# Kernel tuning notes

Hardware: AMD Instinct MI355X
Metric: run time of the kernel (lower is better)

The kernel has to match this reference:

```python
import jax, jax.numpy as jnp
import numpy as np
import math

NEG = -1e9
B, TX, TY, ODIM = 32, 512, 2048, 80


def setup_inputs() -> dict:
    key = jax.random.key(0)
    k1, k2 = jax.random.split(key)
    return {
        "x_m": jax.random.normal(k1, (B, TX, ODIM), jnp.float32),
        "x_logs": jnp.zeros((B, TX, ODIM), jnp.float32),  # mean_only=True -> zeros_like(x_m)
        "z": jax.random.normal(k2, (B, ODIM, TY), jnp.float32),
        "x_mask": jnp.ones((B, 1, TX), jnp.float32),
        "z_mask": jnp.ones((B, 1, TY), jnp.float32),
    }


def maximum_path(logp, mask, tx_len, ty_len):
    """Monotonic alignment search (Glow-TTS Viterbi DP).
    logp: [B, Tx, Ty] log-likelihoods; mask: [B, Tx, Ty]; lengths: [B] int32.
    Returns hard alignment path [B, Tx, Ty] in {0,1}.
    """
    B_, Tx, Ty = logp.shape
    xs = jnp.arange(Tx)
    logp = jnp.where(mask > 0, logp, NEG)

    # Forward DP over mel frames y: f[x,y] = logp[x,y] + max(f[x-1,y-1], f[x,y-1])
    def fwd_step(prev, y):
        v_cur = jnp.where(xs[None, :] == y, NEG, prev)              # stay (invalid on diagonal)
        prev_shift = jnp.concatenate(
            [jnp.full((B_, 1), NEG, logp.dtype), prev[:, :-1]], axis=1)
        v_prev = jnp.where(xs[None, :] == 0,
                           jnp.where(y == 0, jnp.zeros((), logp.dtype), jnp.asarray(NEG, logp.dtype)),
                           prev_shift)                               # advance
        f = logp[:, :, y] + jnp.maximum(v_prev, v_cur)
        return f, f

    _, fcols = jax.lax.scan(fwd_step, jnp.full((B_, Tx), NEG, logp.dtype), jnp.arange(Ty))
    # fcols: [Ty, B, Tx]

    # Backtrack from (tx_len-1, ty_len-1) down to y=0.
    def bwd_step(index, y):
        active = y < ty_len                                          # [B] bool
        row = jax.nn.one_hot(index, Tx, dtype=logp.dtype) * active[:, None].astype(logp.dtype)
        fm1 = fcols[jnp.maximum(y - 1, 0)]                           # [B, Tx]
        f_here = jnp.take_along_axis(fm1, index[:, None], axis=1)[:, 0]
        f_left = jnp.take_along_axis(fm1, jnp.maximum(index - 1, 0)[:, None], axis=1)[:, 0]
        move = (index != 0) & ((index == y) | (f_here < f_left))
        new_index = jnp.where(active & move, index - 1, index)
        return new_index, row

    _, rows = jax.lax.scan(bwd_step, tx_len - 1, jnp.arange(Ty - 1, -1, -1))
    path = jnp.flip(rows, axis=0).transpose(1, 2, 0)                 # [B, Tx, Ty]
    return path * mask


def reference(x_m, x_logs, z, x_mask, z_mask):
    # attn_mask: [B, Tx, Ty]
    attn_mask = x_mask[:, 0, :, None] * z_mask[:, 0, None, :]

    # Gaussian log-likelihood of each frame z[:, :, y] under each text token's N(x_m, exp(x_logs))
    x_s_sq_r = jnp.exp(-2.0 * x_logs)                                # [B, Tx, D]
    logp1 = jnp.sum(-0.5 * math.log(2.0 * math.pi) - x_logs, axis=2)[:, :, None]
    logp2 = jnp.einsum('btd,bdy->bty', x_s_sq_r, -0.5 * z * z)
    logp3 = jnp.einsum('btd,bdy->bty', x_m * x_s_sq_r, z)
    logp4 = jnp.sum(-0.5 * x_m * x_m * x_s_sq_r, axis=2)[:, :, None]
    logp = logp1 + logp2 + logp3 + logp4                             # [B, Tx, Ty]

    tx_len = jnp.sum(x_mask[:, 0, :], axis=1).astype(jnp.int32)
    ty_len = jnp.sum(z_mask[:, 0, :], axis=1).astype(jnp.int32)
    attn = jax.lax.stop_gradient(
        maximum_path(jax.lax.stop_gradient(logp), attn_mask, tx_len, ty_len))

    # Expand token stats to frame level with the hard alignment.
    z_m = jnp.einsum('bxy,bxd->bdy', attn, x_m)                      # [B, D, Ty]
    z_logs = jnp.einsum('bxy,bxd->bdy', attn, x_logs)                # [B, D, Ty]
    log_durations_ = jnp.log(1e-8 + jnp.sum(attn, axis=-1))[:, None, :] * x_mask  # [B, 1, Tx]
    return z_m, z_logs, log_durations_, attn
```

## Files before the change

### kernel.cpp

```cpp
#include <hip/hip_runtime.h>
#include <math.h>

#define B_ 32
#define TX_ 512
#define TY_ 2048
#define D_ 80
#define NEG (-1e9f)
#define SEG 32

typedef float f32x4 __attribute__((ext_vector_type(4)));

#define GLB(p) ((const __attribute__((address_space(1))) void*)(p))
#define LDSP(p) ((__attribute__((address_space(3))) void*)(p))

__global__ __launch_bounds__(128) void prep_kernel(
    const float* __restrict__ x_m, const float* __restrict__ x_logs,
    float* __restrict__ Cc, int* __restrict__ flag)
{
    int row = blockIdx.x;
    int t = threadIdx.x;
    __shared__ float red[128];
    float contrib = 0.f;
    bool nz = false;
    if (t < D_) {
        float xl = x_logs[(size_t)row * D_ + t];
        float xm = x_m[(size_t)row * D_ + t];
        nz = (xl != 0.f);
        float a1 = expf(-2.f * xl);
        contrib = -0.91893853320467274178f - xl - 0.5f * xm * xm * a1;
    }
    unsigned long long m = __ballot(nz);
    if ((t & 63) == 0 && m) atomicOr(flag, 1);
    red[t] = contrib;
    __syncthreads();
    if (t < 64) {
        float v = red[t] + red[t + 64];
        #pragma unroll
        for (int off = 32; off >= 1; off >>= 1) v += __shfl_down(v, off);
        if (t == 0) Cc[row] = v;
    }
}

__global__ __launch_bounds__(256) void lens_kernel(const float* __restrict__ x_mask,
    const float* __restrict__ z_mask, int* __restrict__ lens)
{
    int blk = blockIdx.x; int t = threadIdx.x;
    __shared__ float red[256];
    float s = 0.f;
    if (blk < B_) {
        for (int i = t; i < TX_; i += 256) s += x_mask[(size_t)blk * TX_ + i];
    } else {
        int b = blk - B_;
        for (int i = t; i < TY_; i += 256) s += z_mask[(size_t)b * TY_ + i];
    }
    red[t] = s; __syncthreads();
    for (int off = 128; off >= 1; off >>= 1) {
        if (t < off) red[t] += red[t + off];
        __syncthreads();
    }
    if (t == 0) lens[blk] = (int)(red[0] + 0.5f);
}

__global__ __launch_bounds__(256) void gemm_zero(
    const int* __restrict__ flag,
    const float* __restrict__ x_m, const float* __restrict__ Cc,
    const float* __restrict__ z,
    const float* __restrict__ x_mask, const float* __restrict__ z_mask,
    float* __restrict__ logpT, int y0, int C)
{
    if (*flag != 0) return;
    __shared__ float xs[40][132];
    __shared__ float zs[40][132];
    int b = blockIdx.z;
    int x0 = blockIdx.x * 128;
    int cy0 = blockIdx.y * 128;
    int yy0 = y0 + cy0;
    int tid = threadIdx.x;
    int tm = tid & 15, tn = tid >> 4;
    float acc[8][8];
    float accz[8];
    #pragma unroll
    for (int i = 0; i < 8; ++i) {
        accz[i] = 0.f;
        #pragma unroll
        for (int j = 0; j < 8; ++j) acc[i][j] = 0.f;
    }

    for (int h = 0; h < 2; ++h) {
        if (h) __syncthreads();
        for (int i = tid; i < 128 * 40; i += 256) {
            int m = i / 40, d = i - m * 40;
            xs[d][m] = x_m[((size_t)(b * TX_ + x0 + m)) * D_ + h * 40 + d];
        }
        for (int i = tid; i < 40 * 128; i += 256) {
            int d = i >> 7, n = i & 127;
            zs[d][n] = z[((size_t)(b * D_ + h * 40 + d)) * TY_ + yy0 + n];
        }
        __syncthreads();
        #pragma unroll 4
        for (int k = 0; k < 40; ++k) {
            f32x4 a0 = *(const f32x4*)&xs[k][tm * 4];
            f32x4 a1 = *(const f32x4*)&xs[k][64 + tm * 4];
            f32x4 z0 = *(const f32x4*)&zs[k][tn * 4];
            f32x4 z1 = *(const f32x4*)&zs[k][64 + tn * 4];
            float av[8], zv[8];
            #pragma unroll
            for (int i = 0; i < 4; ++i) { av[i] = a0[i]; av[i+4] = a1[i]; zv[i] = z0[i]; zv[i+4] = z1[i]; }
            #pragma unroll
            for (int j = 0; j < 8; ++j) {
                accz[j] = fmaf(zv[j], zv[j], accz[j]);
                #pragma unroll
                for (int i = 0; i < 8; ++i)
                    acc[i][j] = fmaf(av[i], zv[j], acc[i][j]);
            }
        }
    }
    f32x4 ccA = *(const f32x4*)&Cc[(size_t)b * TX_ + x0 + tm * 4];
    f32x4 ccB = *(const f32x4*)&Cc[(size_t)b * TX_ + x0 + 64 + tm * 4];
    f32x4 xmA = *(const f32x4*)&x_mask[(size_t)b * TX_ + x0 + tm * 4];
    f32x4 xmB = *(const f32x4*)&x_mask[(size_t)b * TX_ + x0 + 64 + tm * 4];
    #pragma unroll
    for (int jj = 0; jj < 8; ++jj) {
        int n = (jj < 4) ? (tn * 4 + jj) : (64 + tn * 4 + (jj - 4));
        float zmv = z_mask[(size_t)b * TY_ + yy0 + n];
        float sz = -0.5f * accz[jj];
        f32x4 oA, oB;
        #pragma unroll
        for (int i = 0; i < 4; ++i) {
            float vA = acc[i][jj] + ccA[i] + sz;
            float vB = acc[i + 4][jj] + ccB[i] + sz;
            oA[i] = (xmA[i] * zmv > 0.f) ? vA : NEG;
            oB[i] = (xmB[i] * zmv > 0.f) ? vB : NEG;
        }
        float* orow = &logpT[((size_t)b * C + cy0 + n) * TX_ + x0];
        *(f32x4*)(orow + tm * 4) = oA;
        *(f32x4*)(orow + 64 + tm * 4) = oB;
    }
}

__global__ __launch_bounds__(256) void gemm_logp(
    const int* __restrict__ flag,
    const float* __restrict__ x_m, const float* __restrict__ x_logs,
    const float* __restrict__ Cc,
    const float* __restrict__ z, const float* __restrict__ x_mask, const float* __restrict__ z_mask,
    float* __restrict__ logpT, int y0, int C)
{
    if (*flag == 0) return;
    __shared__ float A1s[D_][72];
    __shared__ float A2s[D_][72];
    __shared__ float zs[D_][64];
    int b = blockIdx.z;
    int x0 = blockIdx.x * 64;
    int cy0 = blockIdx.y * 64;
    int yy0 = y0 + cy0;
    int tid = threadIdx.x;
    for (int i = tid; i < 64 * D_; i += 256) {
        int m = i / D_, d = i - m * D_;
        size_t ga = ((size_t)(b * TX_ + x0 + m)) * D_ + d;
        float xl = x_logs[ga], xm = x_m[ga];
        float a1 = expf(-2.f * xl);
        A1s[d][m] = a1;
        A2s[d][m] = xm * a1;
    }
    for (int i = tid; i < D_ * 64; i += 256) {
        int d = i >> 6, n = i & 63;
        zs[d][n] = z[((size_t)(b * D_ + d)) * TY_ + yy0 + n];
    }
    __syncthreads();
    int tm = tid & 15, tn = tid >> 4;
    float acc[4][4];
    #pragma unroll
    for (int i = 0; i < 4; ++i)
        #pragma unroll
        for (int j = 0; j < 4; ++j) acc[i][j] = 0.f;
    #pragma unroll 4
    for (int k = 0; k < D_; ++k) {
        f32x4 a1 = *(const f32x4*)&A1s[k][tm * 4];
        f32x4 a2 = *(const f32x4*)&A2s[k][tm * 4];
        f32x4 zv = *(const f32x4*)&zs[k][tn * 4];
        #pragma unroll
        for (int j = 0; j < 4; ++j) {
            float h = -0.5f * zv[j];
            #pragma unroll
            for (int i = 0; i < 4; ++i) {
                float tt = fmaf(h, a1[i], a2[i]);
                acc[i][j] = fmaf(zv[j], tt, acc[i][j]);
            }
        }
    }
    f32x4 cc = *(const f32x4*)&Cc[(size_t)b * TX_ + x0 + tm * 4];
    f32x4 xm = *(const f32x4*)&x_mask[(size_t)b * TX_ + x0 + tm * 4];
    #pragma unroll
    for (int j = 0; j < 4; ++j) {
        int n = tn * 4 + j;
        float zmv = z_mask[(size_t)b * TY_ + yy0 + n];
        f32x4 o;
        #pragma unroll
        for (int i = 0; i < 4; ++i) {
            float val = acc[i][j] + cc[i];
            o[i] = (xm[i] * zmv > 0.f) ? val : NEG;
        }
        *(f32x4*)&logpT[((size_t)b * C + cy0 + n) * TX_ + x0 + tm * 4] = o;
    }
}

__device__ __forceinline__ unsigned int dp_step(int y, int lane, const f32x4 la, const f32x4 lb,
    float (&f)[8], unsigned int laneMask)
{
    float lp8[8];
    #pragma unroll
    for (int i = 0; i < 4; ++i) { lp8[i] = la[i]; lp8[i + 4] = lb[i]; }
    float sh = __shfl_up(f[7], 1);
    float edge = (y == 0) ? 0.f : NEG;
    float pm0 = (lane == 0) ? edge : sh;
    bool lanehit = (lane == (y >> 3));
    int jeq = y & 7;
    unsigned int byt = 0u;
    #pragma unroll
    for (int j = 7; j >= 0; --j) {
        float pm = (j == 0) ? pm0 : f[j - 1];
        bool ceq = lanehit && (jeq == j);
        byt = byt * 2u + (((f[j] < pm) || ceq) ? 1u : 0u);
        float vc = ceq ? NEG : f[j];
        f[j] = lp8[j] + fmaxf(pm, vc);
    }
    return byt & laneMask;
}

__device__ __forceinline__ void stage_seg(const char* gbase, float (*dst)[TX_],
    int sw, int t0)
{
    for (int d = sw; d < 2 * SEG; d += 3) {
        int s = d >> 1, h = d & 1;
        const char* g = gbase + ((size_t)(t0 + s) * TX_ + h * 256) * 4;
        __builtin_amdgcn_global_load_lds(GLB(g), LDSP(&dst[s][h * 256]), 16, 0, 0);
    }
}

__global__ __launch_bounds__(256, 1) void dp_forward(const float* __restrict__ logpT,
    float* __restrict__ fsave, unsigned char* __restrict__ bits8, int y0, int C)
{
    __shared__ float buf[2][SEG][TX_];
    int b = blockIdx.x, tid = threadIdx.x;
    int w = tid >> 6, lane = tid & 63;
    const char* gbase = (const char*)(logpT + (size_t)b * C * TX_) + lane * 16;
    unsigned char* bp = bits8 + ((size_t)b * TY_ + y0) * 64 + lane;

    float f[8];
    unsigned int laneMask = (lane == 0) ? 0xFEu : 0xFFu;
    if (w == 0) {
        if (y0 == 0) {
            #pragma unroll
            for (int j = 0; j < 8; ++j) f[j] = NEG;
        } else {
            f32x4 fa = *(const f32x4*)(fsave + (size_t)b * TX_ + lane * 8);
            f32x4 fb = *(const f32x4*)(fsave + (size_t)b * TX_ + lane * 8 + 4);
            #pragma unroll
            for (int j = 0; j < 4; ++j) { f[j] = fa[j]; f[j + 4] = fb[j]; }
        }
    } else {
        #pragma unroll
        for (int j = 0; j < 8; ++j) f[j] = 0.f;
    }

    if (w > 0) {
        stage_seg(gbase, buf[0], w - 1, 0);
        asm volatile("s_waitcnt vmcnt(0)" ::: "memory");
    }
    __syncthreads();

    int nseg = C / SEG;
    for (int g = 0; g < nseg; ++g) {
        if (w == 0) {
            float (*cur)[TX_] = buf[g & 1];
            int t0 = g * SEG;
            #pragma unroll 8
            for (int s = 0; s < SEG; ++s) {
                f32x4 la = *(const f32x4*)&cur[s][lane * 8];
                f32x4 lb = *(const f32x4*)&cur[s][lane * 8 + 4];
                unsigned int byt = dp_step(y0 + t0 + s, lane, la, lb, f, laneMask);
                bp[(size_t)(t0 + s) * 64] = (unsigned char)byt;
            }
        } else {
            if (g + 1 < nseg) stage_seg(gbase, buf[(g + 1) & 1], w - 1, (g + 1) * SEG);
            asm volatile("s_waitcnt vmcnt(0)" ::: "memory");
        }
        __syncthreads();
    }

    if (w == 0) {
        f32x4 fa, fb;
        #pragma unroll
        for (int j = 0; j < 4; ++j) { fa[j] = f[j]; fb[j] = f[j + 4]; }
        *(f32x4*)(fsave + (size_t)b * TX_ + lane * 8) = fa;
        *(f32x4*)(fsave + (size_t)b * TX_ + lane * 8 + 4) = fb;
    }
}

__global__ __launch_bounds__(64) void backtrack_kernel(
    const unsigned char* __restrict__ bits8, const int* __restrict__ lens,
    const float* __restrict__ x_mask, int* __restrict__ idxA, float* __restrict__ logdur)
{
    int b = blockIdx.x, lane = threadIdx.x;
    __shared__ int durS[TX_];
    for (int x = lane; x < TX_; x += 64) durS[x] = 0;
    int tx_len = lens[b];
    int ty_len = lens[B_ + b];
    int idx = tx_len - 1;
    if (idx < 0) idx = 0;
    int cnt = 0;
    const unsigned long long* bu = (const unsigned long long*)(bits8 + (size_t)b * TY_ * 64);
    for (int w = 0; w < TY_ / 64; ++w) {
        int ytop = TY_ - 1 - w * 64;
        int yl = ytop - lane;
        int Whi = idx >> 6;
        unsigned long long whi = bu[(size_t)yl * 8 + Whi];
        unsigned long long wlo = (Whi > 0) ? bu[(size_t)yl * 8 + Whi - 1] : 0ull;
        int rec = -1;
        for (int s = 0; s < 64; ++s) {
            int y = ytop - s;
            bool active = (y < ty_len);
            if (lane == s) rec = active ? idx : -1;
            if (active) cnt++;
            unsigned long long wsel = ((idx >> 6) == Whi) ? __shfl(whi, s) : __shfl(wlo, s);
            int bit = (int)((wsel >> (idx & 63)) & 1ull);
            if (active && bit) {
                if (lane == 0) durS[idx] = cnt;
                cnt = 0;
                idx -= 1;
            }
        }
        idxA[(size_t)b * TY_ + yl] = rec;
    }
    if (lane == 0) durS[idx] = cnt;
    __syncthreads();
    for (int x = lane; x < TX_; x += 64) {
        float dv = (float)durS[x];
        logdur[(size_t)b * TX_ + x] = logf(1e-8f + dv) * x_mask[(size_t)b * TX_ + x];
    }
}

__global__ __launch_bounds__(256) void attn_write(const int* __restrict__ idxA,
    const float* __restrict__ x_mask, const float* __restrict__ z_mask,
    float* __restrict__ attn_o)
{
    int b = blockIdx.z; int x = blockIdx.y;
    int yq = blockIdx.x * 256 + threadIdx.x;
    int4 iv = ((const int4*)(idxA + (size_t)b * TY_))[yq];
    float xm = x_mask[(size_t)b * TX_ + x];
    float4 zm4 = ((const float4*)(z_mask + (size_t)b * TY_))[yq];
    float4 o;
    o.x = (iv.x == x) ? xm * zm4.x : 0.f;
    o.y = (iv.y == x) ? xm * zm4.y : 0.f;
    o.z = (iv.z == x) ? xm * zm4.z : 0.f;
    o.w = (iv.w == x) ? xm * zm4.w : 0.f;
    ((float4*)(attn_o + ((size_t)(b * TX_ + x)) * TY_))[yq] = o;
}

__global__ __launch_bounds__(256) void zm_write(const int* __restrict__ idxA,
    const float* __restrict__ x_m, const float* __restrict__ x_logs,
    const float* __restrict__ x_mask, const float* __restrict__ z_mask,
    float* __restrict__ z_m_o, float* __restrict__ z_logs_o)
{
    int b = blockIdx.z; int d = blockIdx.y;
    int yq = blockIdx.x * 256 + threadIdx.x;
    int4 iv = ((const int4*)(idxA + (size_t)b * TY_))[yq];
    float4 zm4 = ((const float4*)(z_mask + (size_t)b * TY_))[yq];
    float4 om, ol;
    float* omv = (float*)&om; float* olv = (float*)&ol;
    int ivv[4] = {iv.x, iv.y, iv.z, iv.w};
    float zmv[4] = {zm4.x, zm4.y, zm4.z, zm4.w};
    #pragma unroll
    for (int c = 0; c < 4; ++c) {
        float vm = 0.f, vl = 0.f;
        int ix = ivv[c];
        if (ix >= 0) {
            float wgt = x_mask[(size_t)b * TX_ + ix] * zmv[c];
            size_t ga = ((size_t)(b * TX_ + ix)) * D_ + d;
            vm = wgt * x_m[ga];
            vl = wgt * x_logs[ga];
        }
        omv[c] = vm; olv[c] = vl;
    }
    ((float4*)(z_m_o    + ((size_t)(b * D_ + d)) * TY_))[yq] = om;
    ((float4*)(z_logs_o + ((size_t)(b * D_ + d)) * TY_))[yq] = ol;
}

extern "C" void kernel_launch(void* const* d_in, const int* in_sizes, int n_in,
                              void* d_out, int out_size, void* d_ws, size_t ws_size,
                              hipStream_t stream)
{
    const float* x_m    = (const float*)d_in[0];
    const float* x_logs = (const float*)d_in[1];
    const float* z      = (const float*)d_in[2];
    const float* x_mask = (const float*)d_in[3];
    const float* z_mask = (const float*)d_in[4];
    float* out = (float*)d_out;
    float* z_m_o    = out;
    float* z_logs_o = out + (size_t)B_ * D_ * TY_;
    float* logdur_o = out + (size_t)2 * B_ * D_ * TY_;
    float* attn_o   = logdur_o + (size_t)B_ * TX_;

    char* p = (char*)d_ws;
    float* Cc = (float*)p;            p += (size_t)B_ * TX_ * 4;
    float* fs = (float*)p;            p += (size_t)B_ * TX_ * 4;
    unsigned char* bits8 = (unsigned char*)p; p += (size_t)B_ * TY_ * 64;
    int* idxA = (int*)p;              p += (size_t)B_ * TY_ * 4;
    int* lens = (int*)p;              p += 256;
    int* flag = (int*)p;              p += 256;
    float* logpC = (float*)p;
    size_t fixed = (size_t)(p - (char*)d_ws);
    size_t avail = (ws_size > fixed) ? (ws_size - fixed) : 0;
    int C = 128;
    const int cands[5] = {2048, 1024, 512, 256, 128};
    for (int i = 0; i < 5; ++i) {
        if ((size_t)B_ * cands[i] * TX_ * 4 <= avail) { C = cands[i]; break; }
    }

    hipMemsetAsync(flag, 0, sizeof(int), stream);
    prep_kernel<<<B_ * TX_, 128, 0, stream>>>(x_m, x_logs, Cc, flag);
    lens_kernel<<<2 * B_, 256, 0, stream>>>(x_mask, z_mask, lens);
    int nc = TY_ / C;
    for (int c = 0; c < nc; ++c) {
        gemm_zero<<<dim3(TX_ / 128, C / 128, B_), 256, 0, stream>>>(
            flag, x_m, Cc, z, x_mask, z_mask, logpC, c * C, C);
        gemm_logp<<<dim3(TX_ / 64, C / 64, B_), 256, 0, stream>>>(
            flag, x_m, x_logs, Cc, z, x_mask, z_mask, logpC, c * C, C);
        dp_forward<<<B_, 256, 0, stream>>>(logpC, fs, bits8, c * C, C);
    }
    backtrack_kernel<<<B_, 64, 0, stream>>>(bits8, lens, x_mask, idxA, logdur_o);
    attn_write<<<dim3(TY_ / 4 / 256, TX_, B_), 256, 0, stream>>>(idxA, x_mask, z_mask, attn_o);
    zm_write<<<dim3(TY_ / 4 / 256, D_, B_), 256, 0, stream>>>(
        idxA, x_m, x_logs, x_mask, z_mask, z_m_o, z_logs_o);
}
```

Measured before the change: 761.5 us.

## Stride DP columns across lanes and emit direction bits via wave ballots

The forward DP's cell-to-lane mapping changes from 8 contiguous cells per lane to a strided mapping where lane l owns cells j*64+l. Each step now rotates all 8 register values across lanes with shuffles. This removes the serial 8-deep max chain inside each lane, and the direction bits come from ballots, written as 8 64-bit words by 8 lanes instead of 64 byte stores. The bit layout in memory stays what the backtrack kernel expects. The cost is 8 cross-lane permutes per step instead of 1, plus ballot overhead.

```diff
diff --git a/kernel.cpp b/kernel.cpp
--- a/kernel.cpp
+++ b/kernel.cpp
@@ -204,29 +204,6 @@
     }
 }
 
-__device__ __forceinline__ unsigned int dp_step(int y, int lane, const f32x4 la, const f32x4 lb,
-    float (&f)[8], unsigned int laneMask)
-{
-    float lp8[8];
-    #pragma unroll
-    for (int i = 0; i < 4; ++i) { lp8[i] = la[i]; lp8[i + 4] = lb[i]; }
-    float sh = __shfl_up(f[7], 1);
-    float edge = (y == 0) ? 0.f : NEG;
-    float pm0 = (lane == 0) ? edge : sh;
-    bool lanehit = (lane == (y >> 3));
-    int jeq = y & 7;
-    unsigned int byt = 0u;
-    #pragma unroll
-    for (int j = 7; j >= 0; --j) {
-        float pm = (j == 0) ? pm0 : f[j - 1];
-        bool ceq = lanehit && (jeq == j);
-        byt = byt * 2u + (((f[j] < pm) || ceq) ? 1u : 0u);
-        float vc = ceq ? NEG : f[j];
-        f[j] = lp8[j] + fmaxf(pm, vc);
-    }
-    return byt & laneMask;
-}
-
 __device__ __forceinline__ void stage_seg(const char* gbase, float (*dst)[TX_],
     int sw, int t0)
 {
@@ -244,19 +221,16 @@
     int b = blockIdx.x, tid = threadIdx.x;
     int w = tid >> 6, lane = tid & 63;
     const char* gbase = (const char*)(logpT + (size_t)b * C * TX_) + lane * 16;
-    unsigned char* bp = bits8 + ((size_t)b * TY_ + y0) * 64 + lane;
+    unsigned long long* wp = (unsigned long long*)(bits8 + ((size_t)b * TY_ + y0) * 64);
 
     float f[8];
-    unsigned int laneMask = (lane == 0) ? 0xFEu : 0xFFu;
     if (w == 0) {
         if (y0 == 0) {
             #pragma unroll
             for (int j = 0; j < 8; ++j) f[j] = NEG;
         } else {
-            f32x4 fa = *(const f32x4*)(fsave + (size_t)b * TX_ + lane * 8);
-            f32x4 fb = *(const f32x4*)(fsave + (size_t)b * TX_ + lane * 8 + 4);
             #pragma unroll
-            for (int j = 0; j < 4; ++j) { f[j] = fa[j]; f[j + 4] = fb[j]; }
+            for (int j = 0; j < 8; ++j) f[j] = fsave[(size_t)b * TX_ + j * 64 + lane];
         }
     } else {
         #pragma unroll
@@ -269,17 +243,46 @@
     }
     __syncthreads();
 
+    int rotsrc = (lane + 63) & 63;
     int nseg = C / SEG;
     for (int g = 0; g < nseg; ++g) {
         if (w == 0) {
             float (*cur)[TX_] = buf[g & 1];
             int t0 = g * SEG;
-            #pragma unroll 8
+            #pragma unroll 4
             for (int s = 0; s < SEG; ++s) {
-                f32x4 la = *(const f32x4*)&cur[s][lane * 8];
-                f32x4 lb = *(const f32x4*)&cur[s][lane * 8 + 4];
-                unsigned int byt = dp_step(y0 + t0 + s, lane, la, lb, f, laneMask);
-                bp[(size_t)(t0 + s) * 64] = (unsigned char)byt;
+                int y = y0 + t0 + s;
+                const float* row = &cur[s][0];
+                float lp[8];
+                #pragma unroll
+                for (int j = 0; j < 8; ++j) lp[j] = row[j * 64 + lane];
+                float r[8];
+                #pragma unroll
+                for (int j = 0; j < 8; ++j) r[j] = __shfl(f[j], rotsrc);
+                float edge = (y == 0) ? 0.f : NEG;
+                int jeq = y >> 6;
+                bool lhit = (lane == (y & 63)) && (y < TX_);
+                unsigned long long wrd[8];
+                #pragma unroll
+                for (int j = 0; j < 8; ++j) {
+                    float pm;
+                    if (j == 0) pm = (lane == 0) ? edge : r[0];
+                    else        pm = (lane == 0) ? r[j - 1] : r[j];
+                    bool ceq = lhit && (jeq == j);
+                    bool pred = (f[j] < pm) || ceq;
+                    wrd[j] = __ballot(pred);
+                    float vc = ceq ? NEG : f[j];
+                    f[j] = lp[j] + fmaxf(pm, vc);
+                }
+                wrd[0] &= ~1ull;
+                if (lane < 8) {
+                    unsigned long long wv =
+                        (lane & 4) ? ((lane & 2) ? ((lane & 1) ? wrd[7] : wrd[6])
+                                                 : ((lane & 1) ? wrd[5] : wrd[4]))
+                                   : ((lane & 2) ? ((lane & 1) ? wrd[3] : wrd[2])
+                                                 : ((lane & 1) ? wrd[1] : wrd[0]));
+                    wp[(size_t)(t0 + s) * 8 + lane] = wv;
+                }
             }
         } else {
             if (g + 1 < nseg) stage_seg(gbase, buf[(g + 1) & 1], w - 1, (g + 1) * SEG);
@@ -289,11 +292,8 @@
     }
 
     if (w == 0) {
-        f32x4 fa, fb;
-        #pragma unroll
-        for (int j = 0; j < 4; ++j) { fa[j] = f[j]; fb[j] = f[j + 4]; }
-        *(f32x4*)(fsave + (size_t)b * TX_ + lane * 8) = fa;
-        *(f32x4*)(fsave + (size_t)b * TX_ + lane * 8 + 4) = fb;
+        #pragma unroll
+        for (int j = 0; j < 8; ++j) fsave[(size_t)b * TX_ + j * 64 + lane] = f[j];
     }
 }
 
```

Result: slower. 1.394 ms (+83.1%).
